# Performance work log

Hardware: AMD Instinct MI355X
Metric: run time of the kernel (lower is better)

Reference implementation:

```python
import jax, jax.numpy as jnp
import numpy as np

NEG_SLOPE = 0.2  # PyG GATConv default negative_slope


def setup_inputs() -> dict:
    key = jax.random.key(0)
    k1, k2, k3, k4, k5, k6 = jax.random.split(key, 6)
    N, E, DIN, DOUT = 100000, 1600000, 128, 64
    x = jax.random.normal(k1, (N, DIN), dtype=jnp.float32)
    edge_index = jax.random.randint(k2, (2, E), 0, N, dtype=jnp.int64)
    # learned params (glorot-like scale)
    W = jax.random.normal(k3, (DIN, DOUT), dtype=jnp.float32) * (1.0 / np.sqrt(DIN))
    att_src = jax.random.normal(k4, (DOUT,), dtype=jnp.float32) * (1.0 / np.sqrt(DOUT))
    att_dst = jax.random.normal(k5, (DOUT,), dtype=jnp.float32) * (1.0 / np.sqrt(DOUT))
    bias = jnp.zeros((DOUT,), dtype=jnp.float32)
    return {"x": x, "edge_index": edge_index, "W": W,
            "att_src": att_src, "att_dst": att_dst, "bias": bias}


def reference(x, edge_index, W, att_src, att_dst, bias):
    N = x.shape[0]
    # add self loops (PyG default add_self_loops=True)
    loop = jnp.arange(N, dtype=edge_index.dtype)
    src = jnp.concatenate([edge_index[0], loop])  # message sources (x_j)
    dst = jnp.concatenate([edge_index[1], loop])  # aggregation targets (x_i)

    h = x @ W                         # [N, C] linear transform (heads=1)
    a_src = h @ att_src               # [N] per-node source score
    a_dst = h @ att_dst               # [N] per-node target score

    # per-edge raw attention: LeakyReLU(alpha_j + alpha_i)
    e = jax.nn.leaky_relu(a_src[src] + a_dst[dst], NEG_SLOPE)  # [Etot]

    # segment softmax over edges grouped by destination node
    e_max = jax.ops.segment_max(e, dst, num_segments=N)        # every node has self loop
    e_exp = jnp.exp(e - e_max[dst])
    e_sum = jax.ops.segment_sum(e_exp, dst, num_segments=N)
    alpha = e_exp / (e_sum[dst] + 1e-16)                       # [Etot]

    # weighted scatter-add aggregation
    out = jax.ops.segment_sum(h[src] * alpha[:, None], dst, num_segments=N)
    return out + bias
```

## Files before the change

### kernel.cpp

```cpp
#include <hip/hip_runtime.h>
#include <cstddef>

#define DIN 128
#define DOUT 64
#define BKT_SHIFT 7
#define BKT_NODES 128
#define CAP 2680
#define CAPP 2816
#define MAXB 800
#define EPB 8192
#define TW 784

#define QDEC (0.25f / 32767.f)
#define QENC (32767.f / 0.25f)

typedef __attribute__((ext_vector_type(8))) short bf16x8;
typedef __attribute__((ext_vector_type(4))) float f32x4;

__device__ __forceinline__ float leakyrelu(float v) { return v > 0.f ? v : 0.2f * v; }

__device__ __forceinline__ unsigned cvtpk(float lo, float hi) {
    unsigned r;
    asm volatile("v_cvt_pk_bf16_f32 %0, %1, %2" : "=v"(r) : "v"(lo), "v"(hi));
    return r;
}
__device__ __forceinline__ bf16x8 cvt8(f32x4 lo, f32x4 hi) {
    union { bf16x8 v; unsigned u[4]; } cv;
    cv.u[0] = cvtpk(lo[0], lo[1]);
    cv.u[1] = cvtpk(lo[2], lo[3]);
    cv.u[2] = cvtpk(hi[0], hi[1]);
    cv.u[3] = cvtpk(hi[2], hi[3]);
    return cv.v;
}

__global__ __launch_bounds__(1024) void k_front(
    const float* __restrict__ x, const float* __restrict__ W,
    const float* __restrict__ att_src, const float* __restrict__ att_dst,
    signed char* __restrict__ h8, float2* __restrict__ sa2, float* __restrict__ adst,
    const int* __restrict__ src, const int* __restrict__ dst,
    unsigned int* __restrict__ sorted, int* __restrict__ table,
    int N, int E, int NB, int NBT)
{
    __shared__ unsigned int sbufL[EPB];
    __shared__ int hist[MAXB];
    __shared__ int offA[MAXB + 1];
    const int tid = threadIdx.x;

    if (blockIdx.x < NBT) {
        const int lane = tid & 63, g = lane >> 4, c15 = lane & 15;
        const int n0w = blockIdx.x * 512 + (tid >> 6) * 32;
        if (n0w >= N) return;

        bf16x8 afrag[2][4];
        #pragma unroll
        for (int u = 0; u < 2; ++u) {
            const int arow = min(n0w + u * 16 + c15, N - 1);
            const float* xr = x + (size_t)arow * DIN + g * 8;
            #pragma unroll
            for (int kb = 0; kb < 4; ++kb) {
                f32x4 lo = *reinterpret_cast<const f32x4*>(xr + kb * 32);
                f32x4 hi = *reinterpret_cast<const f32x4*>(xr + kb * 32 + 4);
                afrag[u][kb] = cvt8(lo, hi);
            }
        }

        f32x4 acc[2][4];
        #pragma unroll
        for (int nt = 0; nt < 4; ++nt) {
            f32x4 a0 = {0.f, 0.f, 0.f, 0.f};
            f32x4 a1 = {0.f, 0.f, 0.f, 0.f};
            #pragma unroll
            for (int kb = 0; kb < 4; ++kb) {
                const float* wp = W + (size_t)(kb * 32 + g * 8) * DOUT + nt * 16 + c15;
                f32x4 lo, hi;
                #pragma unroll
                for (int i = 0; i < 4; ++i) lo[i] = wp[i * DOUT];
                #pragma unroll
                for (int i = 0; i < 4; ++i) hi[i] = wp[(i + 4) * DOUT];
                bf16x8 bfr = cvt8(lo, hi);
                a0 = __builtin_amdgcn_mfma_f32_16x16x32_bf16(afrag[0][kb], bfr, a0, 0, 0, 0);
                a1 = __builtin_amdgcn_mfma_f32_16x16x32_bf16(afrag[1][kb], bfr, a1, 0, 0, 0);
            }
            acc[0][nt] = a0;
            acc[1][nt] = a1;
        }

        #pragma unroll
        for (int u = 0; u < 2; ++u) {
            float mr[4];
            #pragma unroll
            for (int r = 0; r < 4; ++r) {
                float m = fabsf(acc[u][0][r]);
                #pragma unroll
                for (int nt = 1; nt < 4; ++nt) m = fmaxf(m, fabsf(acc[u][nt][r]));
                mr[r] = m;
            }
            #pragma unroll
            for (int mask = 1; mask < 16; mask <<= 1)
                #pragma unroll
                for (int r = 0; r < 4; ++r) mr[r] = fmaxf(mr[r], __shfl_xor(mr[r], mask));

            float inv[4];
            #pragma unroll
            for (int r = 0; r < 4; ++r) inv[r] = 127.f / fmaxf(mr[r], 1e-20f);

            #pragma unroll
            for (int nt = 0; nt < 4; ++nt)
                #pragma unroll
                for (int r = 0; r < 4; ++r) {
                    int row = n0w + u * 16 + g * 4 + r;
                    if (row < N) {
                        int qi = __float2int_rn(acc[u][nt][r] * inv[r]);
                        qi = max(-127, min(127, qi));
                        h8[(size_t)row * DOUT + nt * 16 + c15] = (signed char)qi;
                    }
                }

            float ps[4] = {0.f, 0.f, 0.f, 0.f}, pd[4] = {0.f, 0.f, 0.f, 0.f};
            #pragma unroll
            for (int nt = 0; nt < 4; ++nt) {
                float as = att_src[nt * 16 + c15];
                float ad = att_dst[nt * 16 + c15];
                #pragma unroll
                for (int r = 0; r < 4; ++r) {
                    ps[r] = fmaf(acc[u][nt][r], as, ps[r]);
                    pd[r] = fmaf(acc[u][nt][r], ad, pd[r]);
                }
            }
            #pragma unroll
            for (int mask = 1; mask < 16; mask <<= 1)
                #pragma unroll
                for (int r = 0; r < 4; ++r) {
                    ps[r] += __shfl_xor(ps[r], mask);
                    pd[r] += __shfl_xor(pd[r], mask);
                }
            #pragma unroll
            for (int r = 0; r < 4; ++r) {
                int row = n0w + u * 16 + g * 4 + r;
                if (c15 == r && row < N) {
                    sa2[row] = make_float2(ps[r], fmaxf(mr[r], 1e-20f) * (1.f / 127.f));
                    adst[row] = pd[r];
                }
            }
        }
        return;
    }

    const int c = blockIdx.x - NBT;
    const int e0 = c * EPB;
    const int cnt = min(EPB, E - e0);

    for (int i = tid; i < NB; i += 1024) hist[i] = 0;
    __syncthreads();

    unsigned pv[8]; int bv[8], rv[8];
    #pragma unroll
    for (int k = 0; k < 8; ++k) {
        int e = e0 + k * 1024 + tid;
        if (e < E) {
            int d = dst[e];
            pv[k] = (unsigned)src[e] | ((unsigned)(d & (BKT_NODES - 1)) << 17);
            bv[k] = d >> BKT_SHIFT;
            rv[k] = atomicAdd(&hist[bv[k]], 1);
        } else bv[k] = -1;
    }
    __syncthreads();

    if (tid < NB) offA[tid + 1] = hist[tid];
    if (tid == 0) offA[0] = 0;
    __syncthreads();
    for (int st = 1; st < NB; st <<= 1) {
        int add = 0;
        if (tid < NB && tid >= st) add = offA[tid + 1 - st];
        __syncthreads();
        if (tid < NB && tid >= st) offA[tid + 1] += add;
        __syncthreads();
    }

    for (int i = tid; i <= NB; i += 1024) table[(size_t)c * TW + i] = offA[i];

    #pragma unroll
    for (int k = 0; k < 8; ++k)
        if (bv[k] >= 0) sbufL[offA[bv[k]] + rv[k]] = pv[k];
    __syncthreads();

    for (int i = tid; i < cnt; i += 1024)
        sorted[(size_t)c * EPB + i] = sbufL[i];
}

__global__ __launch_bounds__(512) void k_csr(
    const unsigned int* __restrict__ sorted, const int* __restrict__ table,
    const float2* __restrict__ sa2, const float* __restrict__ adst,
    unsigned int* __restrict__ cpk, int2* __restrict__ nspan,
    int N, int NC)
{
    __shared__ unsigned int el[CAP];
    __shared__ float eal[CAP];
    __shared__ int cpre[513];
    __shared__ int hist[BKT_NODES], hist2[BKT_NODES], offs[BKT_NODES + 1];
    __shared__ float ssumL[BKT_NODES], selfC[BKT_NODES], adL[BKT_NODES];

    const int tid = threadIdx.x;
    const int b = blockIdx.x;
    const int n0 = b << BKT_SHIFT;
    const int nn = min(BKT_NODES, N - n0);

    int s0 = 0, len = 0;
    if (tid < NC) {
        s0 = table[(size_t)tid * TW + b];
        len = table[(size_t)tid * TW + b + 1] - s0;
    }
    if (tid < NC) cpre[tid + 1] = len;
    if (tid == 0) cpre[0] = 0;
    __syncthreads();
    for (int st = 1; st < NC; st <<= 1) {
        int add = 0;
        if (tid < NC && tid >= st) add = cpre[tid + 1 - st];
        __syncthreads();
        if (tid < NC && tid >= st) cpre[tid + 1] += add;
        __syncthreads();
    }
    if (tid < NC && len > 0) {
        int d0 = cpre[tid];
        const unsigned int* p = sorted + (size_t)tid * EPB + s0;
        int lim = min(len, CAP - d0);
        for (int i = 0; i < lim; ++i) el[d0 + i] = p[i];
    }
    if (tid < BKT_NODES) { hist[tid] = 0; hist2[tid] = 0; }
    if (tid < nn) {
        int n = n0 + tid;
        float ad = adst[n];
        adL[tid] = ad;
        float2 v = sa2[n];
        float selfA = __expf(leakyrelu(v.x + ad));
        ssumL[tid] = selfA;
        selfC[tid] = selfA * v.y;
    }
    __syncthreads();
    int cnt = cpre[NC]; if (cnt > CAP) cnt = CAP;

    for (int i = tid; i < cnt; i += 512) {
        unsigned int e = el[i];
        int ln = e >> 17;
        float2 vs = sa2[e & 0x1FFFF];
        float a = __expf(leakyrelu(vs.x + adL[ln]));
        eal[i] = a * vs.y;
        atomicAdd(&hist[ln], 1);
        atomicAdd(&ssumL[ln], a);
    }
    __syncthreads();
    if (tid < nn) ssumL[tid] = 1.f / (ssumL[tid] + 1e-16f);

    if (tid < BKT_NODES) offs[tid + 1] = hist[tid] + 1;
    if (tid == 0) offs[0] = 0;
    __syncthreads();
    for (int off = 1; off < BKT_NODES; off <<= 1) {
        int v = 0;
        if (tid < BKT_NODES && tid >= off) v = offs[tid + 1 - off];
        __syncthreads();
        if (tid < BKT_NODES && tid >= off) offs[tid + 1] += v;
        __syncthreads();
    }

    const size_t gbase = (size_t)b * CAPP;
    for (int i = tid; i < cnt; i += 512) {
        unsigned int e = el[i];
        int ln = e >> 17;
        unsigned int s = e & 0x1FFFF;
        int r = atomicAdd(&hist2[ln], 1);
        int p = offs[ln] + r;
        float c = eal[i] * ssumL[ln];
        unsigned q = (unsigned)fminf(c * QENC + 0.5f, 32767.f);
        cpk[gbase + p] = s | (q << 17);
    }
    __syncthreads();

    if (tid < nn) {
        int n = n0 + tid;
        int pend = offs[tid + 1];
        float c = selfC[tid] * ssumL[tid];
        unsigned q = (unsigned)fminf(c * QENC + 0.5f, 32767.f);
        cpk[gbase + pend - 1] = (unsigned)n | (q << 17);
        nspan[n] = make_int2((int)gbase + offs[tid], (int)gbase + pend);
    }
}

__global__ __launch_bounds__(256) void k_agg(
    const int2* __restrict__ nspan, const unsigned int* __restrict__ cpk,
    const signed char* __restrict__ h8, const float* __restrict__ bias,
    float* __restrict__ out, int N)
{
    const int lane = threadIdx.x & 63;
    const int c15 = lane & 15;
    const int grp = lane >> 4;
    const int n = blockIdx.x * 4 + (threadIdx.x >> 6);
    if (n >= N) return;
    const int2 span = nspan[n];
    const int st = span.x, en = span.y;

    const float4 bv = *reinterpret_cast<const float4*>(bias + c15 * 4);

    int acc0 = 0, acc1 = 0, acc2 = 0, acc3 = 0;
    for (int base = st; base < en; base += 32) {
        unsigned mdl = cpk[min(base + (lane & 31), en - 1)];
        unsigned mdq[8]; int qv[8]; unsigned hw[8];
        #pragma unroll
        for (int t = 0; t < 8; ++t) mdq[t] = __shfl(mdl, t * 4 + grp);
        #pragma unroll
        for (int t = 0; t < 8; ++t) {
            int e = base + t * 4 + grp;
            qv[t] = (e < en) ? (int)(mdq[t] >> 17) : 0;
        }
        #pragma unroll
        for (int t = 0; t < 8; ++t)
            hw[t] = *reinterpret_cast<const unsigned*>(
                h8 + (size_t)(mdq[t] & 0x1FFFFu) * DOUT + c15 * 4);
        #pragma unroll
        for (int t = 0; t < 8; ++t) {
            acc0 += __mul24(qv[t], (int)(signed char)(hw[t]));
            acc1 += __mul24(qv[t], (int)(signed char)(hw[t] >> 8));
            acc2 += __mul24(qv[t], (int)(signed char)(hw[t] >> 16));
            acc3 += __mul24(qv[t], (int)(signed char)(hw[t] >> 24));
        }
    }

    acc0 += __shfl_xor(acc0, 16); acc0 += __shfl_xor(acc0, 32);
    acc1 += __shfl_xor(acc1, 16); acc1 += __shfl_xor(acc1, 32);
    acc2 += __shfl_xor(acc2, 16); acc2 += __shfl_xor(acc2, 32);
    acc3 += __shfl_xor(acc3, 16); acc3 += __shfl_xor(acc3, 32);

    if (grp == 0) {
        float4 r;
        r.x = (float)acc0 * QDEC + bv.x;
        r.y = (float)acc1 * QDEC + bv.y;
        r.z = (float)acc2 * QDEC + bv.z;
        r.w = (float)acc3 * QDEC + bv.w;
        *reinterpret_cast<float4*>(out + (size_t)n * DOUT + c15 * 4) = r;
    }
}

extern "C" void kernel_launch(void* const* d_in, const int* in_sizes, int n_in,
                              void* d_out, int out_size, void* d_ws, size_t ws_size,
                              hipStream_t stream)
{
    const float* x       = (const float*)d_in[0];
    const int*   edge    = (const int*)d_in[1];
    const float* W       = (const float*)d_in[2];
    const float* att_src = (const float*)d_in[3];
    const float* att_dst = (const float*)d_in[4];
    const float* bias    = (const float*)d_in[5];

    const int N = in_sizes[0] / DIN;
    const int E = in_sizes[1] / 2;
    const int* src = edge;
    const int* dst = edge + E;
    float* out = (float*)d_out;

    const int NB = (N + BKT_NODES - 1) >> BKT_SHIFT;
    const int NC = (E + EPB - 1) / EPB;
    const int NBT = (N + 511) / 512;

    signed char* h8 = (signed char*)d_ws;
    float2* sa2 = (float2*)(h8 + (size_t)N * DOUT);
    float* adst = (float*)(sa2 + N);
    int2* nspan = (int2*)(adst + N);
    unsigned int* sorted = (unsigned int*)(nspan + N);
    int* table = (int*)(sorted + (size_t)NC * EPB);
    unsigned int* cpk = (unsigned int*)(table + (size_t)NC * TW);

    k_front<<<NBT + NC, 1024, 0, stream>>>(x, W, att_src, att_dst, h8, sa2, adst,
                                           src, dst, sorted, table, N, E, NB, NBT);
    k_csr  <<<NB, 512, 0, stream>>>(sorted, table, sa2, adst, cpk, nspan, N, NC);
    k_agg  <<<(N + 3) / 4, 256, 0, stream>>>(nspan, cpk, h8, bias, out, N);
}
```

Before: 87.20 us.

## Use wave-shuffle block scans, parallel chunk gather, and cached per-edge ranks in CSR build

Replaces the shared-memory Hillis-Steele scans (one barrier pair per step) in k_front and k_csr with a wave-level shuffle scan plus a small cross-wave scan, so each scan needs only two barriers. The serial per-chunk copy into the bucket edge list, where one thread copied a whole chunk, becomes a parallel gather in which each thread binary-searches the chunk prefix array. The per-node rank from the first atomic pass is stored in a byte array and reused, which removes the second atomic histogram pass. The costs are extra shared memory and a binary search per edge, and the byte ranks assume no node has more than 255 incoming edges within a bucket.

```diff
diff --git a/kernel.cpp b/kernel.cpp
--- a/kernel.cpp
+++ b/kernel.cpp
@@ -31,6 +31,31 @@
     cv.u[2] = cvtpk(hi[0], hi[1]);
     cv.u[3] = cvtpk(hi[2], hi[3]);
     return cv.v;
+}
+
+template<int T>
+__device__ __forceinline__ int block_incl_scan(int v, int tid, volatile int* wscr) {
+    int s = v;
+    #pragma unroll
+    for (int d = 1; d < 64; d <<= 1) {
+        int t = __shfl_up(s, d);
+        if ((tid & 63) >= d) s += t;
+    }
+    if ((tid & 63) == 63) wscr[tid >> 6] = s;
+    __syncthreads();
+    constexpr int NW = T / 64;
+    if (tid < NW) {
+        int w = wscr[tid];
+        int sw = w;
+        #pragma unroll
+        for (int d = 1; d < NW; d <<= 1) {
+            int t = __shfl_up(sw, d);
+            if (tid >= d) sw += t;
+        }
+        wscr[tid] = sw - w;
+    }
+    __syncthreads();
+    return s + wscr[tid >> 6];
 }
 
 __global__ __launch_bounds__(1024) void k_front(
@@ -44,6 +69,7 @@
     __shared__ unsigned int sbufL[EPB];
     __shared__ int hist[MAXB];
     __shared__ int offA[MAXB + 1];
+    __shared__ int wscr[16];
     const int tid = threadIdx.x;
 
     if (blockIdx.x < NBT) {
@@ -166,16 +192,13 @@
     }
     __syncthreads();
 
-    if (tid < NB) offA[tid + 1] = hist[tid];
-    if (tid == 0) offA[0] = 0;
-    __syncthreads();
-    for (int st = 1; st < NB; st <<= 1) {
-        int add = 0;
-        if (tid < NB && tid >= st) add = offA[tid + 1 - st];
-        __syncthreads();
-        if (tid < NB && tid >= st) offA[tid + 1] += add;
-        __syncthreads();
-    }
+    {
+        int v = (tid < NB) ? hist[tid] : 0;
+        int incl = block_incl_scan<1024>(v, tid, wscr);
+        if (tid < NB) offA[tid + 1] = incl;
+        if (tid == 0) offA[0] = 0;
+    }
+    __syncthreads();
 
     for (int i = tid; i <= NB; i += 1024) table[(size_t)c * TW + i] = offA[i];
 
@@ -196,37 +219,30 @@
 {
     __shared__ unsigned int el[CAP];
     __shared__ float eal[CAP];
+    __shared__ unsigned char rnk[CAP];
     __shared__ int cpre[513];
-    __shared__ int hist[BKT_NODES], hist2[BKT_NODES], offs[BKT_NODES + 1];
+    __shared__ int cs0[512];
+    __shared__ int hist[BKT_NODES], offs[BKT_NODES + 1];
     __shared__ float ssumL[BKT_NODES], selfC[BKT_NODES], adL[BKT_NODES];
+    __shared__ int wscr[8];
 
     const int tid = threadIdx.x;
     const int b = blockIdx.x;
     const int n0 = b << BKT_SHIFT;
     const int nn = min(BKT_NODES, N - n0);
 
-    int s0 = 0, len = 0;
+    int len = 0;
     if (tid < NC) {
-        s0 = table[(size_t)tid * TW + b];
+        int s0 = table[(size_t)tid * TW + b];
         len = table[(size_t)tid * TW + b + 1] - s0;
-    }
-    if (tid < NC) cpre[tid + 1] = len;
-    if (tid == 0) cpre[0] = 0;
-    __syncthreads();
-    for (int st = 1; st < NC; st <<= 1) {
-        int add = 0;
-        if (tid < NC && tid >= st) add = cpre[tid + 1 - st];
-        __syncthreads();
-        if (tid < NC && tid >= st) cpre[tid + 1] += add;
-        __syncthreads();
-    }
-    if (tid < NC && len > 0) {
-        int d0 = cpre[tid];
-        const unsigned int* p = sorted + (size_t)tid * EPB + s0;
-        int lim = min(len, CAP - d0);
-        for (int i = 0; i < lim; ++i) el[d0 + i] = p[i];
-    }
-    if (tid < BKT_NODES) { hist[tid] = 0; hist2[tid] = 0; }
+        cs0[tid] = s0;
+    }
+    {
+        int incl = block_incl_scan<512>((tid < NC) ? len : 0, tid, wscr);
+        if (tid < NC) cpre[tid + 1] = incl;
+        if (tid == 0) cpre[0] = 0;
+    }
+    if (tid < BKT_NODES) hist[tid] = 0;
     if (tid < nn) {
         int n = n0 + tid;
         float ad = adst[n];
@@ -240,37 +256,43 @@
     int cnt = cpre[NC]; if (cnt > CAP) cnt = CAP;
 
     for (int i = tid; i < cnt; i += 512) {
+        int lo = 0, hi = NC;
+        while (hi - lo > 1) {
+            int mid = (lo + hi) >> 1;
+            if (cpre[mid] <= i) lo = mid; else hi = mid;
+        }
+        el[i] = sorted[(size_t)lo * EPB + cs0[lo] + (i - cpre[lo])];
+    }
+    __syncthreads();
+
+    for (int i = tid; i < cnt; i += 512) {
         unsigned int e = el[i];
         int ln = e >> 17;
         float2 vs = sa2[e & 0x1FFFF];
         float a = __expf(leakyrelu(vs.x + adL[ln]));
         eal[i] = a * vs.y;
-        atomicAdd(&hist[ln], 1);
+        rnk[i] = (unsigned char)atomicAdd(&hist[ln], 1);
         atomicAdd(&ssumL[ln], a);
     }
     __syncthreads();
     if (tid < nn) ssumL[tid] = 1.f / (ssumL[tid] + 1e-16f);
 
-    if (tid < BKT_NODES) offs[tid + 1] = hist[tid] + 1;
-    if (tid == 0) offs[0] = 0;
-    __syncthreads();
-    for (int off = 1; off < BKT_NODES; off <<= 1) {
-        int v = 0;
-        if (tid < BKT_NODES && tid >= off) v = offs[tid + 1 - off];
-        __syncthreads();
-        if (tid < BKT_NODES && tid >= off) offs[tid + 1] += v;
-        __syncthreads();
-    }
+    {
+        int v = (tid < BKT_NODES) ? hist[tid] + 1 : 0;
+        int incl = block_incl_scan<512>(v, tid, wscr);
+        if (tid < BKT_NODES) offs[tid + 1] = incl;
+        if (tid == 0) offs[0] = 0;
+    }
+    __syncthreads();
 
     const size_t gbase = (size_t)b * CAPP;
     for (int i = tid; i < cnt; i += 512) {
         unsigned int e = el[i];
         int ln = e >> 17;
         unsigned int s = e & 0x1FFFF;
-        int r = atomicAdd(&hist2[ln], 1);
-        int p = offs[ln] + r;
-        float c = eal[i] * ssumL[ln];
-        unsigned q = (unsigned)fminf(c * QENC + 0.5f, 32767.f);
+        int p = offs[ln] + (int)rnk[i];
+        float cq = eal[i] * ssumL[ln];
+        unsigned q = (unsigned)fminf(cq * QENC + 0.5f, 32767.f);
         cpk[gbase + p] = s | (q << 17);
     }
     __syncthreads();
@@ -278,8 +300,8 @@
     if (tid < nn) {
         int n = n0 + tid;
         int pend = offs[tid + 1];
-        float c = selfC[tid] * ssumL[tid];
-        unsigned q = (unsigned)fminf(c * QENC + 0.5f, 32767.f);
+        float cq = selfC[tid] * ssumL[tid];
+        unsigned q = (unsigned)fminf(cq * QENC + 0.5f, 32767.f);
         cpk[gbase + pend - 1] = (unsigned)n | (q << 17);
         nspan[n] = make_int2((int)gbase + offs[tid], (int)gbase + pend);
     }
```

Measured after the change: 85.24 us. -2.3%, faster.
